# Optimization experiments

Hardware: AMD Instinct MI355X
Metric: run time of the kernel (lower is better)

Reference implementation:

```python
import jax, jax.numpy as jnp
import numpy as np

B, HRES, WRES, C = 4, 128, 128, 256
HEADS, WIN, SHIFT, HIDDEN = 8, 8, 4, 1024
N = WIN * WIN
EPS = 1e-5

def _rel_pos_index():
    coords = np.stack(np.meshgrid(np.arange(WIN), np.arange(WIN), indexing='ij'))  # 2,w,w
    cf = coords.reshape(2, -1)
    rel = (cf[:, :, None] - cf[:, None, :]).transpose(1, 2, 0)  # N,N,2
    rel[:, :, 0] += WIN - 1
    rel[:, :, 1] += WIN - 1
    rel[:, :, 0] *= 2 * WIN - 1
    return jnp.asarray(rel.sum(-1))  # [N,N] int

REL_IDX = _rel_pos_index()

def _shift_mask():
    img = np.zeros((HRES, WRES))
    cnt = 0
    for hs in (slice(0, -WIN), slice(-WIN, -SHIFT), slice(-SHIFT, None)):
        for ws in (slice(0, -WIN), slice(-WIN, -SHIFT), slice(-SHIFT, None)):
            img[hs, ws] = cnt; cnt += 1
    m = img.reshape(HRES // WIN, WIN, WRES // WIN, WIN).transpose(0, 2, 1, 3).reshape(-1, N)
    am = m[:, None, :] - m[:, :, None]  # nW,N,N
    return jnp.asarray(np.where(am != 0, -100.0, 0.0).astype(np.float32))

ATTN_MASK = _shift_mask()  # [nW, N, N]

def win_part(x):  # [B,H,W,C] -> [B*nW, N, C]
    b, h, w, c = x.shape
    x = x.reshape(b, h // WIN, WIN, w // WIN, WIN, c)
    return x.transpose(0, 1, 3, 2, 4, 5).reshape(-1, N, c)

def win_rev(wins, h, w):  # [B*nW, N, C] -> [B,H,W,C]
    b = wins.shape[0] // ((h // WIN) * (w // WIN))
    x = wins.reshape(b, h // WIN, w // WIN, WIN, WIN, -1)
    return x.transpose(0, 1, 3, 2, 4, 5).reshape(b, h, w, -1)

def ln(x, g, b):
    mu = x.mean(-1, keepdims=True)
    var = ((x - mu) ** 2).mean(-1, keepdims=True)
    return (x - mu) / jnp.sqrt(var + EPS) * g + b

def setup_inputs() -> dict:
    key = jax.random.key(0)
    ks = jax.random.split(key, 10)
    s = 0.02
    return {
        'x': jax.random.normal(ks[0], (B, HRES * WRES, C), jnp.float32),
        'g1': jnp.ones((C,), jnp.float32), 'be1': jnp.zeros((C,), jnp.float32),
        'wq': jax.random.normal(ks[1], (C, C), jnp.float32) * s,
        'bq': jnp.zeros((C,), jnp.float32),
        'wkv': jax.random.normal(ks[2], (C, 2 * C), jnp.float32) * s,
        'bkv': jnp.zeros((2 * C,), jnp.float32),
        'rpb': jax.random.normal(ks[3], ((2 * WIN - 1) ** 2, HEADS), jnp.float32) * s,
        'wo': jax.random.normal(ks[4], (C, C), jnp.float32) * s,
        'bo': jnp.zeros((C,), jnp.float32),
        'g2': jnp.ones((C,), jnp.float32), 'be2': jnp.zeros((C,), jnp.float32),
        'w1': jax.random.normal(ks[5], (C, HIDDEN), jnp.float32) * s,
        'bl1': jnp.zeros((HIDDEN,), jnp.float32),
        'dww': jax.random.normal(ks[6], (3, 3, 1, HIDDEN), jnp.float32) * s,
        'dwb': jnp.zeros((HIDDEN,), jnp.float32),
        'w2': jax.random.normal(ks[7], (HIDDEN, C), jnp.float32) * s,
        'bl2': jnp.zeros((C,), jnp.float32),
    }

def reference(x, g1, be1, wq, bq, wkv, bkv, rpb, wo, bo, g2, be2, w1, bl1, dww, dwb, w2, bl2):
    b, l, c = x.shape
    hd = c // HEADS
    shortcut = x
    h = ln(x, g1, be1).reshape(b, HRES, WRES, c)
    h = jnp.roll(h, (-SHIFT, -SHIFT), axis=(1, 2))  # cyclic shift
    xw = win_part(h)  # [Bn, N, C]
    q = (xw @ wq + bq).reshape(-1, N, HEADS, hd).transpose(0, 2, 1, 3)
    kv = (xw @ wkv + bkv).reshape(-1, N, 2, HEADS, hd).transpose(2, 0, 3, 1, 4)
    k, v = kv[0], kv[1]
    attn = jnp.einsum('bhnd,bhmd->bhnm', q * (hd ** -0.5), k)
    bias = rpb[REL_IDX].transpose(2, 0, 1)  # [heads, N, N]
    attn = attn + bias[None]
    nW = ATTN_MASK.shape[0]
    attn = attn.reshape(b, nW, HEADS, N, N) + ATTN_MASK[None, :, None]
    attn = jax.nn.softmax(attn, axis=-1).reshape(-1, HEADS, N, N)
    out = jnp.einsum('bhnm,bhmd->bnhd', attn, v).reshape(-1, N, c)
    out = out @ wo + bo
    out = win_rev(out, HRES, WRES)
    out = jnp.roll(out, (SHIFT, SHIFT), axis=(1, 2)).reshape(b, l, c)
    x = shortcut + out
    # LeFF: linear -> gelu -> depthwise 3x3 conv -> gelu -> linear
    y = ln(x, g2, be2)
    y = jax.nn.gelu(y @ w1 + bl1, approximate=False)
    y = y.reshape(b, HRES, WRES, HIDDEN)
    y = jax.lax.conv_general_dilated(y, dww, (1, 1), 'SAME',
                                     dimension_numbers=('NHWC', 'HWIO', 'NHWC'),
                                     feature_group_count=HIDDEN) + dwb
    y = jax.nn.gelu(y, approximate=False)
    y = y.reshape(b, l, HIDDEN) @ w2 + bl2
    return x + y
```

## Files before the change

### kernel.cpp

```cpp
#include <hip/hip_runtime.h>
#include <hip/hip_bf16.h>
#include <math.h>

typedef __bf16 bf16;
typedef __bf16 bf16x8 __attribute__((ext_vector_type(8)));
typedef __bf16 bf16x4 __attribute__((ext_vector_type(4)));
typedef float  f32x4  __attribute__((ext_vector_type(4)));

#define HRES 128
#define WRES 128
#define CDIM 256
#define NHEADS 8
#define HD 32
#define NWIN 64
#define LTOK 16384
#define BATCH 4
#define TOK_TOTAL 65536
#define HIDDEN 1024

__device__ __forceinline__ float gelu_exact(float v) {
    return 0.5f * v * (1.0f + erff(v * 0.70710678118654752f));
}

__device__ __forceinline__ void gld16(const bf16* g, bf16* l) {
    __builtin_amdgcn_global_load_lds(
        (const __attribute__((address_space(1))) unsigned int*)g,
        (__attribute__((address_space(3))) unsigned int*)l, 16, 0, 0);
}


__global__ void prep_qkvw(const float* __restrict__ wq, const float* __restrict__ bq,
                          const float* __restrict__ wkv, const float* __restrict__ bkv,
                          bf16* __restrict__ bt, float* __restrict__ bias) {
    int idx = blockIdx.x * 256 + threadIdx.x;
    int c = idx >> 8, k = idx & 255;
    float v = (c < 256) ? wq[k * 256 + c] : wkv[k * 512 + (c - 256)];
    bt[idx] = (bf16)v;
    if (k == 0) bias[c] = (c < 256) ? bq[c] : bkv[c - 256];
}

__global__ void prep_wt(const float* __restrict__ w, bf16* __restrict__ wt, int K, int N) {
    int idx = blockIdx.x * 256 + threadIdx.x;
    if (idx >= K * N) return;
    int n = idx / K, k = idx - n * K;
    wt[idx] = (bf16)w[(size_t)k * N + n];
}

__global__ void prep_btab(const float* __restrict__ rpb, float* __restrict__ btab) {
    int idx = blockIdx.x * 256 + threadIdx.x;
    int h = idx >> 12;
    int n = (idx >> 6) & 63;
    int m = idx & 63;
    int i1 = n >> 3, j1 = n & 7, i2 = m >> 3, j2 = m & 7;
    int rel = (i1 - i2 + 7) * 15 + (j1 - j2 + 7);
    btab[idx] = rpb[rel * NHEADS + h];
}


__global__ void ln1_winpart(const float* __restrict__ x, const float* __restrict__ g,
                            const float* __restrict__ be, bf16* __restrict__ xw) {
    int wv = (blockIdx.x * blockDim.x + threadIdx.x) >> 6;
    int lane = threadIdx.x & 63;
    int bw = wv >> 6, n = wv & 63;
    int b = bw >> 8, w = bw & 255;
    int wh = w >> 4, ww = w & 15;
    int i = n >> 3, j = n & 7;
    int ph = (wh * 8 + i + 4) & 127, pw = (ww * 8 + j + 4) & 127;
    const float* row = x + ((size_t)(b * LTOK + ph * 128 + pw)) * CDIM;
    float4 v = *(const float4*)(row + lane * 4);
    float s = v.x + v.y + v.z + v.w;
    float ss = v.x * v.x + v.y * v.y + v.z * v.z + v.w * v.w;
    #pragma unroll
    for (int m = 1; m < 64; m <<= 1) { s += __shfl_xor(s, m); ss += __shfl_xor(ss, m); }
    float mu = s * (1.0f / 256.0f);
    float var = ss * (1.0f / 256.0f) - mu * mu;
    float inv = rsqrtf(var + 1e-5f);
    int c0 = lane * 4;
    bf16x4 o;
    o[0] = (bf16)((v.x - mu) * inv * g[c0 + 0] + be[c0 + 0]);
    o[1] = (bf16)((v.y - mu) * inv * g[c0 + 1] + be[c0 + 1]);
    o[2] = (bf16)((v.z - mu) * inv * g[c0 + 2] + be[c0 + 2]);
    o[3] = (bf16)((v.w - mu) * inv * g[c0 + 3] + be[c0 + 3]);
    *(bf16x4*)(xw + (size_t)wv * CDIM + c0) = o;
}

__global__ void ln2_kernel(const float* __restrict__ x2, const float* __restrict__ g,
                           const float* __restrict__ be, bf16* __restrict__ y) {
    int t = (blockIdx.x * blockDim.x + threadIdx.x) >> 6;
    int lane = threadIdx.x & 63;
    const float* row = x2 + (size_t)t * CDIM;
    float4 v = *(const float4*)(row + lane * 4);
    float s = v.x + v.y + v.z + v.w;
    float ss = v.x * v.x + v.y * v.y + v.z * v.z + v.w * v.w;
    #pragma unroll
    for (int m = 1; m < 64; m <<= 1) { s += __shfl_xor(s, m); ss += __shfl_xor(ss, m); }
    float mu = s * (1.0f / 256.0f);
    float var = ss * (1.0f / 256.0f) - mu * mu;
    float inv = rsqrtf(var + 1e-5f);
    int c0 = lane * 4;
    bf16x4 o;
    o[0] = (bf16)((v.x - mu) * inv * g[c0 + 0] + be[c0 + 0]);
    o[1] = (bf16)((v.y - mu) * inv * g[c0 + 1] + be[c0 + 1]);
    o[2] = (bf16)((v.z - mu) * inv * g[c0 + 2] + be[c0 + 2]);
    o[3] = (bf16)((v.w - mu) * inv * g[c0 + 3] + be[c0 + 3]);
    *(bf16x4*)(y + (size_t)t * CDIM + c0) = o;
}

template <int EPI>
__global__ __launch_bounds__(256) void gemm_bt(
    const bf16* __restrict__ A, const bf16* __restrict__ Bt,
    const float* __restrict__ bias, int M, int N, int K, int row0,
    bf16* __restrict__ outb, float* __restrict__ outf, const float* __restrict__ add_f32,
    bf16* __restrict__ qb, bf16* __restrict__ kb, bf16* __restrict__ vtb)
{
    __shared__ bf16 As[128][64];
    __shared__ bf16 Bs[128][64];
    int tid = threadIdx.x;
    int lane = tid & 63;
    int wid = tid >> 6;
    int bm = blockIdx.x * 128, bn = blockIdx.y * 128;
    int wm = (wid >> 1) * 64, wn = (wid & 1) * 64;
    int l15 = lane & 15, l4 = lane >> 4;
    f32x4 acc[4][4] = {};

    const bf16* Abase = A + (size_t)bm * K;
    const bf16* Bbase = Bt + (size_t)bn * K;

    for (int k0 = 0; k0 < K; k0 += 64) {
        #pragma unroll
        for (int it = 0; it < 4; ++it) {
            int e = (it * 256 + tid) * 8;
            int r = e >> 6, kk = e & 63;
            gld16(Abase + (size_t)r * K + k0 + kk, &As[0][0] + e);
            gld16(Bbase + (size_t)r * K + k0 + kk, &Bs[0][0] + e);
        }
        __syncthreads();
        #pragma unroll
        for (int kh = 0; kh < 2; ++kh) {
            bf16x8 af[4], bfr[4];
            #pragma unroll
            for (int mf = 0; mf < 4; ++mf) af[mf]  = *(const bf16x8*)(&As[wm + mf * 16 + l15][kh * 32 + 8 * l4]);
            #pragma unroll
            for (int nf = 0; nf < 4; ++nf) bfr[nf] = *(const bf16x8*)(&Bs[wn + nf * 16 + l15][kh * 32 + 8 * l4]);
            #pragma unroll
            for (int mf = 0; mf < 4; ++mf)
                #pragma unroll
                for (int nf = 0; nf < 4; ++nf)
                    acc[mf][nf] = __builtin_amdgcn_mfma_f32_16x16x32_bf16(af[mf], bfr[nf], acc[mf][nf], 0, 0, 0);
        }
        __syncthreads();
    }

    #pragma unroll
    for (int mf = 0; mf < 4; ++mf)
      #pragma unroll
      for (int nf = 0; nf < 4; ++nf)
        #pragma unroll
        for (int r = 0; r < 4; ++r) {
            int row = bm + wm + mf * 16 + l4 * 4 + r;
            int col = bn + wn + nf * 16 + l15;
            float v = acc[mf][nf][r] + bias[col];
            if constexpr (EPI == 0) {
                int bw_ = row >> 6, n_ = row & 63;
                if (col < 256) {
                    float q = v * 0.17677669529663687f;
                    int h = col >> 5, d = col & 31;
                    qb[(((size_t)bw_ * 8 + h) * 64 + n_) * 32 + d] = (bf16)q;
                } else if (col < 512) {
                    int c2 = col - 256; int h = c2 >> 5, d = c2 & 31;
                    kb[(((size_t)bw_ * 8 + h) * 64 + n_) * 32 + d] = (bf16)v;
                } else {
                    int c2 = col - 512; int h = c2 >> 5, d = c2 & 31;
                    vtb[(((size_t)bw_ * 8 + h) * 32 + d) * 64 + n_] = (bf16)v;
                }
            } else if constexpr (EPI == 1) {
                int bw_ = row >> 6, n_ = row & 63;
                int b = bw_ >> 8, w = bw_ & 255;
                int wh = w >> 4, ww = w & 15;
                int ii = n_ >> 3, jj = n_ & 7;
                int ph = (wh * 8 + ii + 4) & 127, pw = (ww * 8 + jj + 4) & 127;
                size_t gidx = ((size_t)(b * LTOK + ph * 128 + pw)) * CDIM + col;
                outf[gidx] = add_f32[gidx] + v;
            } else if constexpr (EPI == 2) {
                outb[(size_t)row * N + col] = (bf16)gelu_exact(v);
            } else {
                size_t gidx = (size_t)(row0 + row) * N + col;
                outf[gidx] = v + add_f32[gidx];
            }
        }
}

__global__ __launch_bounds__(256) void attn_kernel(
    const bf16* __restrict__ qb, const bf16* __restrict__ kb, const bf16* __restrict__ vtb,
    const float* __restrict__ btab, bf16* __restrict__ ao)
{
    __shared__ bf16 P[4][64][72];
    int wid = threadIdx.x >> 6, lane = threadIdx.x & 63;
    int pair = blockIdx.x * 4 + wid;
    int bw = pair >> 3, h = pair & 7;
    int l15 = lane & 15, l4 = lane >> 4;
    const bf16* Q  = qb  + ((size_t)bw * 8 + h) * 64 * 32;
    const bf16* Kp = kb  + ((size_t)bw * 8 + h) * 64 * 32;
    const bf16* Vt = vtb + ((size_t)bw * 8 + h) * 32 * 64;

    bf16x8 aq[4], bk[4];
    #pragma unroll
    for (int mf = 0; mf < 4; ++mf) aq[mf] = *(const bf16x8*)(Q  + (mf * 16 + l15) * 32 + 8 * l4);
    #pragma unroll
    for (int nf = 0; nf < 4; ++nf) bk[nf] = *(const bf16x8*)(Kp + (nf * 16 + l15) * 32 + 8 * l4);
    f32x4 s[4][4] = {};
    #pragma unroll
    for (int mf = 0; mf < 4; ++mf)
        #pragma unroll
        for (int nf = 0; nf < 4; ++nf)
            s[mf][nf] = __builtin_amdgcn_mfma_f32_16x16x32_bf16(aq[mf], bk[nf], s[mf][nf], 0, 0, 0);

    int w = bw & 255, wh = w >> 4, ww = w & 15;
    int ccode[4];
    #pragma unroll
    for (int nf = 0; nf < 4; ++nf) {
        int m_ = nf * 16 + l15;
        int hc = (wh == 15) ? (((m_ >> 3) < 4) ? 1 : 2) : 0;
        int wc = (ww == 15) ? (((m_ & 7) < 4) ? 1 : 2) : 0;
        ccode[nf] = hc * 3 + wc;
    }
    float rs[4][4];
    #pragma unroll
    for (int mf = 0; mf < 4; ++mf) {
        #pragma unroll
        for (int r = 0; r < 4; ++r) {
            int n_ = mf * 16 + l4 * 4 + r;
            int hc = (wh == 15) ? (((n_ >> 3) < 4) ? 1 : 2) : 0;
            int wc = (ww == 15) ? (((n_ & 7) < 4) ? 1 : 2) : 0;
            int rcode = hc * 3 + wc;
            float sv[4];
            float mx = -1e30f;
            #pragma unroll
            for (int nf = 0; nf < 4; ++nf) {
                int m_ = nf * 16 + l15;
                float t = s[mf][nf][r] + btab[(h * 64 + n_) * 64 + m_];
                if (ccode[nf] != rcode) t -= 100.0f;
                sv[nf] = t;
                mx = fmaxf(mx, t);
            }
            #pragma unroll
            for (int msk = 1; msk < 16; msk <<= 1) mx = fmaxf(mx, __shfl_xor(mx, msk));
            float sum = 0.0f;
            #pragma unroll
            for (int nf = 0; nf < 4; ++nf) { sv[nf] = __expf(sv[nf] - mx); sum += sv[nf]; }
            #pragma unroll
            for (int msk = 1; msk < 16; msk <<= 1) sum += __shfl_xor(sum, msk);
            rs[mf][r] = sum;
            #pragma unroll
            for (int nf = 0; nf < 4; ++nf) P[wid][n_][nf * 16 + l15] = (bf16)sv[nf];
        }
    }
    __syncthreads();

    f32x4 o[4][2] = {};
    #pragma unroll
    for (int kf = 0; kf < 2; ++kf) {
        bf16x8 bv[2];
        #pragma unroll
        for (int nf = 0; nf < 2; ++nf) bv[nf] = *(const bf16x8*)(Vt + (nf * 16 + l15) * 64 + kf * 32 + 8 * l4);
        #pragma unroll
        for (int mf = 0; mf < 4; ++mf) {
            bf16x8 pa = *(const bf16x8*)(&P[wid][mf * 16 + l15][kf * 32 + 8 * l4]);
            #pragma unroll
            for (int nf = 0; nf < 2; ++nf)
                o[mf][nf] = __builtin_amdgcn_mfma_f32_16x16x32_bf16(pa, bv[nf], o[mf][nf], 0, 0, 0);
        }
    }
    #pragma unroll
    for (int mf = 0; mf < 4; ++mf)
      #pragma unroll
      for (int nf = 0; nf < 2; ++nf)
        #pragma unroll
        for (int r = 0; r < 4; ++r) {
            int n_ = mf * 16 + l4 * 4 + r;
            int d = nf * 16 + l15;
            float val = o[mf][nf][r] / rs[mf][r];
            ao[((size_t)bw * 64 + n_) * CDIM + h * 32 + d] = (bf16)val;
        }
}

__global__ void dwconv_kernel(const bf16* __restrict__ h1, const float* __restrict__ dww,
                              const float* __restrict__ dwb, bf16* __restrict__ h2, int pix0) {
    int gid = blockIdx.x * 256 + threadIdx.x;
    int c8 = (gid & 127) * 8;
    int lpix = gid >> 7;
    int pix = pix0 + lpix;
    int b = pix >> 14, p = pix & 16383;
    int ph = p >> 7, pw = p & 127;
    float acc[8];
    #pragma unroll
    for (int j = 0; j < 8; ++j) acc[j] = dwb[c8 + j];
    #pragma unroll
    for (int dy = -1; dy <= 1; ++dy) {
        int y = ph + dy;
        if ((unsigned)y >= 128u) continue;
        #pragma unroll
        for (int dx = -1; dx <= 1; ++dx) {
            int x = pw + dx;
            if ((unsigned)x >= 128u) continue;
            int ln_ = b * LTOK + y * 128 + x - pix0;
            bf16x8 v = *(const bf16x8*)(h1 + (size_t)ln_ * HIDDEN + c8);
            const float* wp = dww + ((dy + 1) * 3 + (dx + 1)) * HIDDEN + c8;
            #pragma unroll
            for (int j = 0; j < 8; ++j) acc[j] += (float)v[j] * wp[j];
        }
    }
    bf16x8 o;
    #pragma unroll
    for (int j = 0; j < 8; ++j) o[j] = (bf16)gelu_exact(acc[j]);
    *(bf16x8*)(h2 + (size_t)lpix * HIDDEN + c8) = o;
}

extern "C" void kernel_launch(void* const* d_in, const int* in_sizes, int n_in,
                              void* d_out, int out_size, void* d_ws, size_t ws_size,
                              hipStream_t stream) {
    const float* x    = (const float*)d_in[0];
    const float* g1   = (const float*)d_in[1];
    const float* be1  = (const float*)d_in[2];
    const float* wq   = (const float*)d_in[3];
    const float* bq   = (const float*)d_in[4];
    const float* wkv  = (const float*)d_in[5];
    const float* bkv  = (const float*)d_in[6];
    const float* rpb  = (const float*)d_in[7];
    const float* wo   = (const float*)d_in[8];
    const float* bo   = (const float*)d_in[9];
    const float* g2   = (const float*)d_in[10];
    const float* be2  = (const float*)d_in[11];
    const float* w1   = (const float*)d_in[12];
    const float* bl1  = (const float*)d_in[13];
    const float* dww  = (const float*)d_in[14];
    const float* dwb  = (const float*)d_in[15];
    const float* w2   = (const float*)d_in[16];
    const float* bl2  = (const float*)d_in[17];
    float* out = (float*)d_out;

    char* ws = (char*)d_ws;
    bf16*  wqkvt  = (bf16*)(ws + 0);
    float* biasq  = (float*)(ws + 393216);
    bf16*  wot    = (bf16*)(ws + 396288);
    bf16*  w1t    = (bf16*)(ws + 527360);
    bf16*  w2t    = (bf16*)(ws + 1051648);
    float* btab   = (float*)(ws + 1575936);
    char*  R1     = ws + 1707008;
    char*  R2     = ws + 1707008 + 100663296;

    bf16*  qb   = (bf16*)(R1 + 0);
    bf16*  kb   = (bf16*)(R1 + 33554432);
    bf16*  vtb  = (bf16*)(R1 + 67108864);
    bf16*  yln  = (bf16*)(R1 + 0);
    bf16*  h2c  = (bf16*)(R1 + 33554432);

    bf16*  ao   = (bf16*)(R2 + 0);
    bf16*  h1c  = (bf16*)(R2 + 0);

    bf16*  xw   = (bf16*)d_out;
    float* x2   = (float*)d_out;

    prep_qkvw<<<768, 256, 0, stream>>>(wq, bq, wkv, bkv, wqkvt, biasq);
    prep_wt<<<256, 256, 0, stream>>>(wo, wot, 256, 256);
    prep_wt<<<1024, 256, 0, stream>>>(w1, w1t, 256, 1024);
    prep_wt<<<1024, 256, 0, stream>>>(w2, w2t, 1024, 256);
    prep_btab<<<128, 256, 0, stream>>>(rpb, btab);

    ln1_winpart<<<16384, 256, 0, stream>>>(x, g1, be1, xw);

    gemm_bt<0><<<dim3(512, 6), 256, 0, stream>>>(xw, wqkvt, biasq, TOK_TOTAL, 768, 256, 0,
                                                 nullptr, nullptr, nullptr, qb, kb, vtb);
    attn_kernel<<<2048, 256, 0, stream>>>(qb, kb, vtb, btab, ao);

    gemm_bt<1><<<dim3(512, 2), 256, 0, stream>>>(ao, wot, bo, TOK_TOTAL, 256, 256, 0,
                                                 nullptr, x2, x, nullptr, nullptr, nullptr);
    ln2_kernel<<<16384, 256, 0, stream>>>(x2, g2, be2, yln);

    for (int c = 0; c < 2; ++c) {
        int pix0 = c * 32768;
        gemm_bt<2><<<dim3(256, 8), 256, 0, stream>>>(yln + (size_t)pix0 * CDIM, w1t, bl1,
                                                     32768, HIDDEN, 256, 0,
                                                     h1c, nullptr, nullptr, nullptr, nullptr, nullptr);
        dwconv_kernel<<<16384, 256, 0, stream>>>(h1c, dww, dwb, h2c, pix0);
        gemm_bt<3><<<dim3(256, 2), 256, 0, stream>>>(h2c, w2t, bl2, 32768, 256, HIDDEN, pix0,
                                                     nullptr, x2, x2, nullptr, nullptr, nullptr);
    }
}
```

Measured before the change: 673.6 us.

## Double-buffer GEMM LDS tiles with async prefetch and XOR swizzle

The bf16 GEMM kernel now keeps two LDS buffers per operand and issues the global-to-LDS loads for the next K tile before computing on the current one, waiting with explicit vmcnt counts instead of a full sync. LDS rows are also XOR-swizzled on both store and read to cut bank conflicts on the fragment loads. This doubles LDS use to 64KB per block, which may lower occupancy. It also relies on hand-written waitcnt and barrier placement being correct.

Result: faster. 646.7 us (-4.0%).

```diff
diff --git a/kernel.cpp b/kernel.cpp
--- a/kernel.cpp
+++ b/kernel.cpp
@@ -113,8 +113,8 @@
     bf16* __restrict__ outb, float* __restrict__ outf, const float* __restrict__ add_f32,
     bf16* __restrict__ qb, bf16* __restrict__ kb, bf16* __restrict__ vtb)
 {
-    __shared__ bf16 As[128][64];
-    __shared__ bf16 Bs[128][64];
+    __shared__ bf16 As[2][128][64];
+    __shared__ bf16 Bs[2][128][64];
     int tid = threadIdx.x;
     int lane = tid & 63;
     int wid = tid >> 6;
@@ -126,29 +126,51 @@
     const bf16* Abase = A + (size_t)bm * K;
     const bf16* Bbase = Bt + (size_t)bn * K;
 
-    for (int k0 = 0; k0 < K; k0 += 64) {
+    auto stage = [&](int b, int k0) {
         #pragma unroll
         for (int it = 0; it < 4; ++it) {
             int e = (it * 256 + tid) * 8;
-            int r = e >> 6, kk = e & 63;
-            gld16(Abase + (size_t)r * K + k0 + kk, &As[0][0] + e);
-            gld16(Bbase + (size_t)r * K + k0 + kk, &Bs[0][0] + e);
-        }
-        __syncthreads();
+            int r = e >> 6, kks = e & 63;
+            int kk = kks ^ ((r & 7) << 3);
+            gld16(Abase + (size_t)r * K + k0 + kk, &As[b][0][0] + e);
+            gld16(Bbase + (size_t)r * K + k0 + kk, &Bs[b][0][0] + e);
+        }
+    };
+
+    int nt = K >> 6;
+    stage(0, 0);
+    int cur = 0;
+    for (int t = 0; t < nt; ++t) {
+        if (t + 1 < nt) {
+            stage(cur ^ 1, (t + 1) << 6);
+            asm volatile("s_waitcnt vmcnt(8)" ::: "memory");
+        } else {
+            asm volatile("s_waitcnt vmcnt(0)" ::: "memory");
+        }
+        __builtin_amdgcn_s_barrier();
+        __builtin_amdgcn_sched_barrier(0);
         #pragma unroll
         for (int kh = 0; kh < 2; ++kh) {
             bf16x8 af[4], bfr[4];
-            #pragma unroll
-            for (int mf = 0; mf < 4; ++mf) af[mf]  = *(const bf16x8*)(&As[wm + mf * 16 + l15][kh * 32 + 8 * l4]);
-            #pragma unroll
-            for (int nf = 0; nf < 4; ++nf) bfr[nf] = *(const bf16x8*)(&Bs[wn + nf * 16 + l15][kh * 32 + 8 * l4]);
+            int col = kh * 32 + 8 * l4;
+            #pragma unroll
+            for (int mf = 0; mf < 4; ++mf) {
+                int row = wm + mf * 16 + l15;
+                af[mf] = *(const bf16x8*)(&As[cur][0][0] + row * 64 + (col ^ ((row & 7) << 3)));
+            }
+            #pragma unroll
+            for (int nf = 0; nf < 4; ++nf) {
+                int row = wn + nf * 16 + l15;
+                bfr[nf] = *(const bf16x8*)(&Bs[cur][0][0] + row * 64 + (col ^ ((row & 7) << 3)));
+            }
             #pragma unroll
             for (int mf = 0; mf < 4; ++mf)
                 #pragma unroll
                 for (int nf = 0; nf < 4; ++nf)
                     acc[mf][nf] = __builtin_amdgcn_mfma_f32_16x16x32_bf16(af[mf], bfr[nf], acc[mf][nf], 0, 0, 0);
         }
-        __syncthreads();
+        __builtin_amdgcn_s_barrier();
+        cur ^= 1;
     }
 
     #pragma unroll
```
